# Kernel tuning notes

Measured on AMD Instinct MI355X. Metric: run time of the kernel, lower is better.

The kernel has to match this reference:

```python
import jax, jax.numpy as jnp
import numpy as np

N_HEADS = 16

def setup_inputs() -> dict:
    key = jax.random.key(0)
    ks = jax.random.split(key, 9)
    B, L, D = 4, 2048, 1024
    s = D ** -0.5
    return {
        "x": jax.random.normal(ks[0], (B, L, D), dtype=jnp.float32),
        "Wq": jax.random.normal(ks[1], (D, D), dtype=jnp.float32) * s,
        "bq": jax.random.normal(ks[2], (D,), dtype=jnp.float32) * 0.02,
        "Wk": jax.random.normal(ks[3], (D, D), dtype=jnp.float32) * s,
        "bk": jax.random.normal(ks[4], (D,), dtype=jnp.float32) * 0.02,
        "Wv": jax.random.normal(ks[5], (D, D), dtype=jnp.float32) * s,
        "bv": jax.random.normal(ks[6], (D,), dtype=jnp.float32) * 0.02,
        "Wo": jax.random.normal(ks[7], (D, D), dtype=jnp.float32) * s,
        "bo": jax.random.normal(ks[8], (D,), dtype=jnp.float32) * 0.02,
    }

def reference(x, Wq, bq, Wk, bk, Wv, bv, Wo, bo):
    B, L, D = x.shape
    H = N_HEADS
    hd = D // H
    scale = hd ** -0.5
    # torch Linear: y = x @ W.T + b
    q = (x @ Wq.T + bq).reshape(B, L, H, hd)
    k = (x @ Wk.T + bk).reshape(B, L, H, hd)
    v = (x @ Wv.T + bv).reshape(B, L, H, hd)
    # scores [B,H,L,L]
    qk = jnp.einsum('bqhd,bkhd->bhqk', q, k) * scale
    causal = jnp.tril(jnp.ones((L, L), dtype=bool))
    qk = jnp.where(causal[None, None, :, :], qk, -jnp.inf)
    attn = jax.nn.softmax(qk, axis=-1)
    out = jnp.einsum('bhqk,bkhd->bqhd', attn, v).reshape(B, L, D)
    return out @ Wo.T + bo
```

## Files before the change

### kernel.cpp

```cpp
#include <hip/hip_runtime.h>
#include <hip/hip_bf16.h>
#include <math.h>

#define Bsz 4
#define Lsz 2048
#define Dsz 1024
#define Hn 16
#define HDsz 64
#define NQT 16

typedef __attribute__((ext_vector_type(8))) short short8;
typedef __attribute__((ext_vector_type(4))) float floatx4;
typedef unsigned short ushort_t;

__device__ __forceinline__ void load_lds_16B(const void* g, void* l) {
    __builtin_amdgcn_global_load_lds(
        (const __attribute__((address_space(1))) unsigned int*)g,
        (__attribute__((address_space(3))) unsigned int*)l, 16, 0, 0);
}

__device__ inline void cvt_store(float* p, size_t i, float v) { p[i] = v; }
__device__ inline void cvt_store(__hip_bfloat16* p, size_t i, float v) {
    p[i] = __float2bfloat16(v);
}

__device__ inline ushort_t f2bf_raw(float f) {
    __hip_bfloat16 b = __float2bfloat16(f);
    return *reinterpret_cast<ushort_t*>(&b);
}

__device__ inline float bf2f_raw(ushort_t u) {
    union { unsigned int i; float f; } c;
    c.i = ((unsigned int)u) << 16;
    return c.f;
}

__device__ __forceinline__ float fast_exp2(float x) {
#if __has_builtin(__builtin_amdgcn_exp2f)
    return __builtin_amdgcn_exp2f(x);
#else
    return exp2f(x);
#endif
}

__device__ __forceinline__ unsigned pk_bf16_rhu(float p0, float p1) {
    return __builtin_amdgcn_perm(__builtin_bit_cast(unsigned, p1) + 0x8000u,
                                 __builtin_bit_cast(unsigned, p0) + 0x8000u,
                                 0x07060302u);
}

__global__ __launch_bounds__(256) void f2b(const float* __restrict__ in,
                                           __hip_bfloat16* __restrict__ out,
                                           int n) {
    int i = (blockIdx.x * 256 + threadIdx.x) * 4;
    if (i >= n) return;
    float4 v = *(const float4*)(in + i);
    out[i + 0] = __float2bfloat16(v.x);
    out[i + 1] = __float2bfloat16(v.y);
    out[i + 2] = __float2bfloat16(v.z);
    out[i + 3] = __float2bfloat16(v.w);
}

__global__ __launch_bounds__(256) void f2b4(const float* __restrict__ w0,
                                            const float* __restrict__ w1,
                                            const float* __restrict__ w2,
                                            const float* __restrict__ w3,
                                            __hip_bfloat16* __restrict__ out) {
    int bid = blockIdx.x;
    int sel = bid >> 10;
    const float* in = sel == 0 ? w0 : (sel == 1 ? w1 : (sel == 2 ? w2 : w3));
    size_t off = (size_t)(bid & 1023) * 1024 + threadIdx.x * 4;
    float4 v = *(const float4*)(in + off);
    __hip_bfloat16* o = out + (size_t)sel * (1024 * 1024) + off;
    o[0] = __float2bfloat16(v.x);
    o[1] = __float2bfloat16(v.y);
    o[2] = __float2bfloat16(v.z);
    o[3] = __float2bfloat16(v.w);
}

template <typename TO, bool QKV>
__global__ __launch_bounds__(512, 2) void gemm_bt_256(
    const ushort_t* __restrict__ A, const ushort_t* __restrict__ W,
    const float* __restrict__ b0, const float* __restrict__ b1,
    const float* __restrict__ b2, TO* __restrict__ C, int M, int N, int K) {
    __shared__ ushort_t As[2][256 * 64];
    __shared__ ushort_t Bs[2][256 * 64];

    const int t = threadIdx.x;
    const int wave = t >> 6, lane = t & 63;
    const int lmod = lane & 15, quad = lane >> 4;
    const int wm = wave >> 2, wn = wave & 3;

    const int nbn = N >> 8;
    const int nwg = nbn * (M >> 8);
    const int bid = blockIdx.x;
    const int wg = (bid & 7) * (nwg >> 3) + (bid >> 3);
    const int n0 = (wg % nbn) * 256, m0 = (wg / nbn) * 256;

    floatx4 acc[2][2][4][2] = {};
    short8 Af[4][2], Bf[2][2];

    const int NT = K >> 6;

    auto stageA = [&](int kt, int bi) {
        const int kk = kt << 6;
#pragma unroll
        for (int p = 0; p < 4; p++) {
            int slot = t + p * 512;
            int row = slot >> 3, c8 = slot & 7;
            int gc8 = c8 ^ (row & 7);
            load_lds_16B(A + (size_t)(m0 + row) * K + kk + gc8 * 8,
                         &As[bi][slot * 8]);
        }
    };
    auto stageB = [&](int kt, int bi) {
        const int kk = kt << 6;
#pragma unroll
        for (int p = 0; p < 4; p++) {
            int slot = t + p * 512;
            int row = slot >> 3, c8 = slot & 7;
            int gc8 = c8 ^ (row & 7);
            load_lds_16B(W + (size_t)(n0 + row) * K + kk + gc8 * 8,
                         &Bs[bi][slot * 8]);
        }
    };
    auto rdA = [&](int bi, int mh) {
#pragma unroll
        for (int mr = 0; mr < 4; mr++) {
            int row = wm * 128 + mh * 64 + mr * 16 + lmod;
#pragma unroll
            for (int ks = 0; ks < 2; ks++) {
                int sc8 = (ks * 4 + quad) ^ (row & 7);
                Af[mr][ks] = *(const short8*)&As[bi][row * 64 + sc8 * 8];
            }
        }
    };
    auto rdB = [&](int bi, int nh) {
#pragma unroll
        for (int nr = 0; nr < 2; nr++) {
            int row = wn * 64 + nh * 32 + nr * 16 + lmod;
#pragma unroll
            for (int ks = 0; ks < 2; ks++) {
                int sc8 = (ks * 4 + quad) ^ (row & 7);
                Bf[nr][ks] = *(const short8*)&Bs[bi][row * 64 + sc8 * 8];
            }
        }
    };
    auto domm = [&](int mh, int nh) {
        __builtin_amdgcn_s_setprio(1);
#pragma unroll
        for (int mr = 0; mr < 4; mr++)
#pragma unroll
            for (int nr = 0; nr < 2; nr++)
#pragma unroll
                for (int ks = 0; ks < 2; ks++)
                    acc[mh][nh][mr][nr] =
                        __builtin_amdgcn_mfma_f32_16x16x32_bf16(
                            Af[mr][ks], Bf[nr][ks], acc[mh][nh][mr][nr], 0, 0,
                            0);
        __builtin_amdgcn_s_setprio(0);
    };

    stageA(0, 0);
    stageB(0, 0);
    asm volatile("s_waitcnt vmcnt(0)" ::: "memory");
    __builtin_amdgcn_s_barrier();
    asm volatile("" ::: "memory");

#pragma unroll 1
    for (int T = 0; T < NT; T++) {
        const int cur = T & 1, nxt = cur ^ 1;
        const bool pf = (T + 1 < NT);
        rdA(cur, 0);
        rdB(cur, 0);
        if (pf) stageA(T + 1, nxt);
        __builtin_amdgcn_s_barrier();
        __builtin_amdgcn_sched_barrier(0);
        domm(0, 0);
        __builtin_amdgcn_s_barrier();
        rdB(cur, 1);
        if (pf) stageB(T + 1, nxt);
        __builtin_amdgcn_s_barrier();
        __builtin_amdgcn_sched_barrier(0);
        domm(0, 1);
        __builtin_amdgcn_s_barrier();
        rdA(cur, 1);
        __builtin_amdgcn_s_barrier();
        __builtin_amdgcn_sched_barrier(0);
        domm(1, 1);
        __builtin_amdgcn_s_barrier();
        rdB(cur, 0);
        __builtin_amdgcn_s_barrier();
        __builtin_amdgcn_sched_barrier(0);
        domm(1, 0);
        asm volatile("s_waitcnt vmcnt(0)" ::: "memory");
        __builtin_amdgcn_s_barrier();
        asm volatile("" ::: "memory");
    }

    const int sec = QKV ? (n0 >> 10) : 0;
    const float* bp = QKV ? (sec == 0 ? b0 : (sec == 1 ? b1 : b2)) : b0;
    TO* Cb = QKV ? (C + (size_t)sec * M * 1024) : C;
    const int Nout = QKV ? 1024 : N;
    const float sc = (QKV && sec == 0) ? 0.1803368801111204f : 1.0f;

#pragma unroll
    for (int mh = 0; mh < 2; mh++)
#pragma unroll
        for (int mr = 0; mr < 4; mr++) {
            int gm = m0 + wm * 128 + mh * 64 + mr * 16 + quad * 4;
#pragma unroll
            for (int nh = 0; nh < 2; nh++)
#pragma unroll
                for (int nr = 0; nr < 2; nr++) {
                    int gn = n0 + wn * 64 + nh * 32 + nr * 16 + lmod;
                    int cn = QKV ? (gn & 1023) : gn;
                    float b = bp[cn];
#pragma unroll
                    for (int r = 0; r < 4; r++)
                        cvt_store(Cb, (size_t)(gm + r) * Nout + cn,
                                  (acc[mh][nh][mr][nr][r] + b) * sc);
                }
        }
}

template <typename TO, bool QKV>
__global__ __launch_bounds__(256) void gemm_bt_mfma(
    const ushort_t* __restrict__ A, const ushort_t* __restrict__ W,
    const float* __restrict__ b0, const float* __restrict__ b1,
    const float* __restrict__ b2, TO* __restrict__ C, int M, int N, int K) {
    __shared__ ushort_t As[128 * 32];
    __shared__ ushort_t Bs[128 * 32];

    const int t = threadIdx.x;
    const int wave = t >> 6, lane = t & 63;

    const int nbx = N >> 7;
    const int nwg = nbx * (M >> 7);
    const int bid = blockIdx.x;
    const int wg = (bid & 7) * (nwg >> 3) + (bid >> 3);
    const int n0 = (wg % nbx) * 128, m0 = (wg / nbx) * 128;

    const int wm = (wave & 1) * 64, wn = (wave >> 1) * 64;
    const int lmod = lane & 15, quad = lane >> 4;

    floatx4 acc[4][4] = {};

    for (int k0 = 0; k0 < K; k0 += 32) {
#pragma unroll
        for (int p = 0; p < 2; p++) {
            int chunk = t + p * 256;
            int r = chunk >> 2;
            int c8 = (chunk & 3) * 8;
            load_lds_16B(A + (size_t)(m0 + r) * K + k0 + c8, &As[chunk * 8]);
            load_lds_16B(W + (size_t)(n0 + r) * K + k0 + c8, &Bs[chunk * 8]);
        }
        __syncthreads();

        short8 af[4], bf_[4];
#pragma unroll
        for (int i = 0; i < 4; i++) {
            af[i] = *(const short8*)&As[(wm + i * 16 + lmod) * 32 + quad * 8];
            bf_[i] = *(const short8*)&Bs[(wn + i * 16 + lmod) * 32 + quad * 8];
        }
#pragma unroll
        for (int i = 0; i < 4; i++)
#pragma unroll
            for (int j = 0; j < 4; j++)
                acc[i][j] = __builtin_amdgcn_mfma_f32_16x16x32_bf16(
                    af[i], bf_[j], acc[i][j], 0, 0, 0);
        __syncthreads();
    }

    const int sec = n0 >> 10;
    const float* bp = QKV ? (sec == 0 ? b0 : (sec == 1 ? b1 : b2)) : b0;
    TO* Cb = QKV ? (C + (size_t)sec * M * 1024) : C;
    const int Nout = QKV ? 1024 : N;
    const float sc = (QKV && sec == 0) ? 0.1803368801111204f : 1.0f;

#pragma unroll
    for (int i = 0; i < 4; i++) {
        int gm = m0 + wm + i * 16 + quad * 4;
#pragma unroll
        for (int j = 0; j < 4; j++) {
            int gn = n0 + wn + j * 16 + lmod;
            int cn = QKV ? (gn & 1023) : gn;
            float b = bp[cn];
#pragma unroll
            for (int r = 0; r < 4; r++)
                cvt_store(Cb, (size_t)(gm + r) * Nout + cn,
                          (acc[i][j][r] + b) * sc);
        }
    }
}

__global__ __launch_bounds__(256) void attn_mfma(
    const ushort_t* __restrict__ q, const ushort_t* __restrict__ k,
    const ushort_t* __restrict__ v, ushort_t* __restrict__ Opart,
    float* __restrict__ lpart) {
    __shared__ ushort_t Ks[64 * 64];
    __shared__ ushort_t Vts[64 * 64];
    __shared__ ushort_t Ps[4][32 * 64];

    const int t = threadIdx.x;
    const int wave = t >> 6, lane = t & 63;
    const int lmod = lane & 15, quad = lane >> 4;

    const int bid = blockIdx.x;
    const int j = bid >> 3;
    const int bx = j & 15;
    const int p = bx & 7, s = bx >> 3;
    const int bh = (bid & 7) + ((j >> 4) << 3);
    const int b = bh >> 4, h = bh & 15;
    const size_t base = ((size_t)b * Lsz) * Dsz + h * HDsz;

    const int vrp = t & 31, vcg = t >> 5;
    ushort_t* Pw = (ushort_t*)Ps[wave];
    const int lm7 = lmod & 7;

#pragma unroll 1
    for (int seg = 0; seg < 2; seg++) {
        const int qtile = seg == 0 ? (NQT - 1 - p) : p;
        const int q0 = qtile * 128;
        const int Th = qtile + 1;
        const int kt0 = s * Th, kt1 = kt0 + Th;

        short8 aq[2][2];
#pragma unroll
        for (int g = 0; g < 2; g++) {
            const ushort_t* qp = q + base +
                                 (size_t)(q0 + wave * 32 + g * 16 + lmod) * Dsz +
                                 quad * 8;
            aq[g][0] = *(const short8*)(qp);
            aq[g][1] = *(const short8*)(qp + 32);
        }

        floatx4 Oacc[2][4] = {};
        float lsum[2] = {0.f, 0.f};

        for (int kt = kt0; kt < kt1; kt++) {
            __syncthreads();

#pragma unroll
            for (int pp = 0; pp < 2; pp++) {
                int slot = t + pp * 256;
                int row = slot >> 3, c8 = slot & 7;
                int gc8 = c8 ^ (row & 7);
                load_lds_16B(k + base + (size_t)(kt * 64 + row) * Dsz + gc8 * 8,
                             &Ks[slot * 8]);
            }
            {
                const ushort_t* v0p =
                    v + base + (size_t)(kt * 64 + 2 * vrp) * Dsz + vcg * 8;
                uint4 v0 = *(const uint4*)v0p;
                uint4 v1 = *(const uint4*)(v0p + Dsz);
                unsigned vv0[4] = {v0.x, v0.y, v0.z, v0.w};
                unsigned vv1[4] = {v1.x, v1.y, v1.z, v1.w};
                const int kk = 2 * vrp;
                const int kc8 = kk >> 3, klo = kk & 7;
#pragma unroll
                for (int jj = 0; jj < 4; jj++) {
                    int d0 = vcg * 8 + 2 * jj;
                    unsigned lo =
                        __builtin_amdgcn_perm(vv1[jj], vv0[jj], 0x05040100u);
                    unsigned hi =
                        __builtin_amdgcn_perm(vv1[jj], vv0[jj], 0x07060302u);
                    *(unsigned*)&Vts[d0 * 64 + (kc8 ^ (d0 & 7)) * 8 + klo] = lo;
                    int d1 = d0 + 1;
                    *(unsigned*)&Vts[d1 * 64 + (kc8 ^ (d1 & 7)) * 8 + klo] = hi;
                }
            }
            __syncthreads();

            floatx4 St[2][4] = {};
#pragma unroll
            for (int nt = 0; nt < 4; nt++) {
                int key = nt * 16 + lmod;
#pragma unroll
                for (int ks = 0; ks < 2; ks++) {
                    int sc8 = (ks * 4 + quad) ^ (key & 7);
                    short8 kf = *(const short8*)&Ks[(key * 8 + sc8) * 8];
#pragma unroll
                    for (int g = 0; g < 2; g++)
                        St[g][nt] = __builtin_amdgcn_mfma_f32_16x16x32_bf16(
                            kf, aq[g][ks], St[g][nt], 0, 0, 0);
                }
            }

            const bool need_mask = (kt >= 2 * qtile);
#pragma unroll
            for (int g = 0; g < 2; g++) {
                int qg = q0 + wave * 32 + g * 16 + lmod;
#pragma unroll
                for (int nt = 0; nt < 4; nt++) {
                    int k0g = kt * 64 + nt * 16 + quad * 4;
                    float p0 = fast_exp2(St[g][nt][0]);
                    float p1 = fast_exp2(St[g][nt][1]);
                    float p2 = fast_exp2(St[g][nt][2]);
                    float p3 = fast_exp2(St[g][nt][3]);
                    if (need_mask) {
                        if (k0g + 0 > qg) p0 = 0.f;
                        if (k0g + 1 > qg) p1 = 0.f;
                        if (k0g + 2 > qg) p2 = 0.f;
                        if (k0g + 3 > qg) p3 = 0.f;
                    }
                    lsum[g] += ((p0 + p1) + (p2 + p3));
                    uint2 w;
                    w.x = pk_bf16_rhu(p0, p1);
                    w.y = pk_bf16_rhu(p2, p3);
                    int c8 = nt * 2 + (quad >> 1);
                    int sc8 = c8 ^ lm7;
                    *(uint2*)&Pw[((g * 16 + lmod) * 8 + sc8) * 8 +
                                 (quad & 1) * 4] = w;
                }
            }

            short8 ap[2][2];
#pragma unroll
            for (int g = 0; g < 2; g++)
#pragma unroll
                for (int ks = 0; ks < 2; ks++) {
                    int sc8 = (ks * 4 + quad) ^ lm7;
                    ap[g][ks] =
                        *(const short8*)&Pw[((g * 16 + lmod) * 8 + sc8) * 8];
                }
#pragma unroll
            for (int on = 0; on < 4; on++) {
                int d = on * 16 + lmod;
#pragma unroll
                for (int ks = 0; ks < 2; ks++) {
                    int sc8 = (ks * 4 + quad) ^ (d & 7);
                    short8 bv = *(const short8*)&Vts[(d * 8 + sc8) * 8];
#pragma unroll
                    for (int g = 0; g < 2; g++)
                        Oacc[g][on] = __builtin_amdgcn_mfma_f32_16x16x32_bf16(
                            ap[g][ks], bv, Oacc[g][on], 0, 0, 0);
                }
            }
        }

#pragma unroll
        for (int g = 0; g < 2; g++) {
            lsum[g] += __shfl_xor(lsum[g], 16);
            lsum[g] += __shfl_xor(lsum[g], 32);
        }

        const size_t rec = ((size_t)bh * NQT + qtile) * 2 + s;
        ushort_t* Orec = Opart + rec * (128 * 64);
        float* lrec = lpart + rec * 128;
#pragma unroll
        for (int g = 0; g < 2; g++) {
            if (quad == 0) lrec[wave * 32 + g * 16 + lmod] = lsum[g];
#pragma unroll
            for (int r = 0; r < 4; r++) {
                int row = wave * 32 + g * 16 + quad * 4 + r;
#pragma unroll
                for (int on = 0; on < 4; on++) {
                    int d = on * 16 + lmod;
                    Orec[row * 64 + d] = f2bf_raw(Oacc[g][on][r]);
                }
            }
        }
    }
}

__global__ __launch_bounds__(256) void attn_combine(
    const ushort_t* __restrict__ Opart, const float* __restrict__ lpart,
    ushort_t* __restrict__ ao) {
    int gidx = blockIdx.x * 256 + threadIdx.x;
    int rowglob = gidx >> 3;
    int c8 = (gidx & 7) * 8;
    int bh = rowglob >> 11;
    int r11 = rowglob & 2047;
    int qtile = r11 >> 7, row = r11 & 127;

    size_t rec0 = ((size_t)bh * NQT + qtile) * 2;
    const ushort_t* O0 = Opart + (rec0 + 0) * (128 * 64) + row * 64 + c8;
    const ushort_t* O1 = Opart + (rec0 + 1) * (128 * 64) + row * 64 + c8;
    float l = lpart[(rec0 + 0) * 128 + row] + lpart[(rec0 + 1) * 128 + row];
    float inv = 1.0f / l;

    short8 a = *(const short8*)O0;
    short8 bvec = *(const short8*)O1;
    short8 o;
#pragma unroll
    for (int j = 0; j < 8; j++) {
        float vv = (bf2f_raw((ushort_t)a[j]) + bf2f_raw((ushort_t)bvec[j])) * inv;
        o[j] = (short)f2bf_raw(vv);
    }
    int b = bh >> 4, h = bh & 15;
    int qg = qtile * 128 + row;
    *(short8*)&ao[((size_t)(b * Lsz + qg)) * Dsz + h * HDsz + c8] = o;
}

extern "C" void kernel_launch(void* const* d_in, const int* in_sizes, int n_in,
                              void* d_out, int out_size, void* d_ws,
                              size_t ws_size, hipStream_t stream) {
    const size_t elems = (size_t)Bsz * Lsz * Dsz;
    const size_t welem = (size_t)Dsz * Dsz;
    const size_t nrec = (size_t)Bsz * Hn * NQT * 2;
    const size_t opart_e = nrec * 128 * 64;
    const size_t need = (5 * elems + 4 * welem + opart_e) * 2 + nrec * 128 * 4;
    if (ws_size < need) return;

    const float* x = (const float*)d_in[0];
    const float* Wq = (const float*)d_in[1];
    const float* bq = (const float*)d_in[2];
    const float* Wk = (const float*)d_in[3];
    const float* bk = (const float*)d_in[4];
    const float* Wv = (const float*)d_in[5];
    const float* bv = (const float*)d_in[6];
    const float* Wo = (const float*)d_in[7];
    const float* bo = (const float*)d_in[8];
    float* out = (float*)d_out;

    __hip_bfloat16* xb = (__hip_bfloat16*)d_ws;
    __hip_bfloat16* q = xb + elems;
    __hip_bfloat16* k = q + elems;
    __hip_bfloat16* v = k + elems;
    __hip_bfloat16* ao = v + elems;
    __hip_bfloat16* Wqb = ao + elems;
    __hip_bfloat16* Wkb = Wqb + welem;
    __hip_bfloat16* Wvb = Wkb + welem;
    __hip_bfloat16* Wob = Wvb + welem;
    ushort_t* Opart = (ushort_t*)(Wob + welem);
    float* lpart = (float*)(Opart + opart_e);

    const int M = Bsz * Lsz, N = Dsz, K = Dsz;

    f2b<<<(int)(elems / 4 + 255) / 256, 256, 0, stream>>>(x, xb, (int)elems);
    f2b4<<<4096, 256, 0, stream>>>(Wq, Wk, Wv, Wo, Wqb);

    gemm_bt_256<__hip_bfloat16, true><<<(3 * N / 256) * (M / 256), 512, 0,
                                        stream>>>(
        (const ushort_t*)xb, (const ushort_t*)Wqb, bq, bk, bv, q, M, 3 * N, K);

    attn_mfma<<<16 * Bsz * Hn, 256, 0, stream>>>(
        (const ushort_t*)q, (const ushort_t*)k, (const ushort_t*)v, Opart,
        lpart);

    attn_combine<<<(int)(elems / 8 / 256), 256, 0, stream>>>(Opart, lpart,
                                                             (ushort_t*)ao);

    gemm_bt_mfma<float, false><<<N / 128 * (M / 128), 256, 0, stream>>>(
        (const ushort_t*)ao, (const ushort_t*)Wob, bo, bo, bo, out, M, N, K);
}
```

Baseline: 282.3 us.

## Double-buffer K tiles and prefetch V into registers in causal attention loop

Splits the K shared-memory tile into two buffers and issues the async global-to-LDS load for the next key tile right after the barrier, so it overlaps the current tile's QK and PV MFMA work. V for the next tile is loaded into registers in the middle of the iteration and written transposed into LDS at the start of the next one. The prefetch crosses the segment boundary into the second query tile. This hides global-load latency that was previously exposed between barriers, at the cost of more LDS, more registers and hand-managed waitcnt/barrier sequencing.

```diff
diff --git a/kernel.cpp b/kernel.cpp
--- a/kernel.cpp
+++ b/kernel.cpp
@@ -298,7 +298,7 @@
     const ushort_t* __restrict__ q, const ushort_t* __restrict__ k,
     const ushort_t* __restrict__ v, ushort_t* __restrict__ Opart,
     float* __restrict__ lpart) {
-    __shared__ ushort_t Ks[64 * 64];
+    __shared__ ushort_t Ks[2][64 * 64];
     __shared__ ushort_t Vts[64 * 64];
     __shared__ ushort_t Ps[4][32 * 64];
 
@@ -318,12 +318,54 @@
     ushort_t* Pw = (ushort_t*)Ps[wave];
     const int lm7 = lmod & 7;
 
+    auto stageK = [&](int kt, int bi) {
+#pragma unroll
+        for (int pp = 0; pp < 2; pp++) {
+            int slot = t + pp * 256;
+            int row = slot >> 3, c8 = slot & 7;
+            int gc8 = c8 ^ (row & 7);
+            load_lds_16B(k + base + (size_t)(kt * 64 + row) * Dsz + gc8 * 8,
+                         &Ks[bi][slot * 8]);
+        }
+    };
+    auto loadV = [&](int kt, uint4& r0, uint4& r1) {
+        const ushort_t* v0p =
+            v + base + (size_t)(kt * 64 + 2 * vrp) * Dsz + vcg * 8;
+        r0 = *(const uint4*)v0p;
+        r1 = *(const uint4*)(v0p + Dsz);
+    };
+    auto writeV = [&](uint4 r0, uint4 r1) {
+        unsigned vv0[4] = {r0.x, r0.y, r0.z, r0.w};
+        unsigned vv1[4] = {r1.x, r1.y, r1.z, r1.w};
+        const int kk = 2 * vrp;
+        const int kc8 = kk >> 3, klo = kk & 7;
+#pragma unroll
+        for (int jj = 0; jj < 4; jj++) {
+            int d0 = vcg * 8 + 2 * jj;
+            unsigned lo = __builtin_amdgcn_perm(vv1[jj], vv0[jj], 0x05040100u);
+            unsigned hi = __builtin_amdgcn_perm(vv1[jj], vv0[jj], 0x07060302u);
+            *(unsigned*)&Vts[d0 * 64 + (kc8 ^ (d0 & 7)) * 8 + klo] = lo;
+            int d1 = d0 + 1;
+            *(unsigned*)&Vts[d1 * 64 + (kc8 ^ (d1 & 7)) * 8 + klo] = hi;
+        }
+    };
+
+    int bi = 0;
+    uint4 vr0, vr1;
+
+    {
+        const int kt00 = s * (NQT - p);
+        stageK(kt00, 0);
+        loadV(kt00, vr0, vr1);
+    }
+
 #pragma unroll 1
     for (int seg = 0; seg < 2; seg++) {
         const int qtile = seg == 0 ? (NQT - 1 - p) : p;
         const int q0 = qtile * 128;
         const int Th = qtile + 1;
         const int kt0 = s * Th, kt1 = kt0 + Th;
+        const int kt0n = s * (p + 1);
 
         short8 aq[2][2];
 #pragma unroll
@@ -338,39 +380,19 @@
         floatx4 Oacc[2][4] = {};
         float lsum[2] = {0.f, 0.f};
 
+#pragma unroll 1
         for (int kt = kt0; kt < kt1; kt++) {
-            __syncthreads();
-
-#pragma unroll
-            for (int pp = 0; pp < 2; pp++) {
-                int slot = t + pp * 256;
-                int row = slot >> 3, c8 = slot & 7;
-                int gc8 = c8 ^ (row & 7);
-                load_lds_16B(k + base + (size_t)(kt * 64 + row) * Dsz + gc8 * 8,
-                             &Ks[slot * 8]);
-            }
-            {
-                const ushort_t* v0p =
-                    v + base + (size_t)(kt * 64 + 2 * vrp) * Dsz + vcg * 8;
-                uint4 v0 = *(const uint4*)v0p;
-                uint4 v1 = *(const uint4*)(v0p + Dsz);
-                unsigned vv0[4] = {v0.x, v0.y, v0.z, v0.w};
-                unsigned vv1[4] = {v1.x, v1.y, v1.z, v1.w};
-                const int kk = 2 * vrp;
-                const int kc8 = kk >> 3, klo = kk & 7;
-#pragma unroll
-                for (int jj = 0; jj < 4; jj++) {
-                    int d0 = vcg * 8 + 2 * jj;
-                    unsigned lo =
-                        __builtin_amdgcn_perm(vv1[jj], vv0[jj], 0x05040100u);
-                    unsigned hi =
-                        __builtin_amdgcn_perm(vv1[jj], vv0[jj], 0x07060302u);
-                    *(unsigned*)&Vts[d0 * 64 + (kc8 ^ (d0 & 7)) * 8 + klo] = lo;
-                    int d1 = d0 + 1;
-                    *(unsigned*)&Vts[d1 * 64 + (kc8 ^ (d1 & 7)) * 8 + klo] = hi;
-                }
-            }
-            __syncthreads();
+            asm volatile("s_waitcnt vmcnt(0)" ::: "memory");
+            __builtin_amdgcn_s_barrier();
+            asm volatile("" ::: "memory");
+
+            writeV(vr0, vr1);
+            asm volatile("s_waitcnt lgkmcnt(0)" ::: "memory");
+            __builtin_amdgcn_s_barrier();
+            asm volatile("" ::: "memory");
+
+            const int ktn = (kt + 1 < kt1) ? kt + 1 : (seg == 0 ? kt0n : -1);
+            if (ktn >= 0) stageK(ktn, bi ^ 1);
 
             floatx4 St[2][4] = {};
 #pragma unroll
@@ -379,7 +401,7 @@
 #pragma unroll
                 for (int ks = 0; ks < 2; ks++) {
                     int sc8 = (ks * 4 + quad) ^ (key & 7);
-                    short8 kf = *(const short8*)&Ks[(key * 8 + sc8) * 8];
+                    short8 kf = *(const short8*)&Ks[bi][(key * 8 + sc8) * 8];
 #pragma unroll
                     for (int g = 0; g < 2; g++)
                         St[g][nt] = __builtin_amdgcn_mfma_f32_16x16x32_bf16(
@@ -415,6 +437,8 @@
                 }
             }
 
+            if (ktn >= 0) loadV(ktn, vr0, vr1);
+
             short8 ap[2][2];
 #pragma unroll
             for (int g = 0; g < 2; g++)
@@ -437,6 +461,8 @@
                             ap[g][ks], bv, Oacc[g][on], 0, 0, 0);
                 }
             }
+
+            bi ^= 1;
         }
 
 #pragma unroll
```

New measurement: 282.2 us. Within noise of the previous version (-0.1%).
